# Optimization experiments

Measured on AMD Instinct MI355X. Metric: run time of the kernel, lower is better.

The kernel has to match this reference:

```python
import jax, jax.numpy as jnp
import numpy as np

TOPK = 10
NUM_CLASSES = 80
ALPHA = 1.0
BETA = 6.0
EPS = 1e-8


def setup_inputs() -> dict:
    key = jax.random.key(0)
    ks = jax.random.split(key, 6)
    B, A, NB, C = 32, 8400, 32, 80
    pred_scores = jax.random.uniform(ks[0], (B, A, C), dtype=jnp.float32)
    # anchor grid for 640x640 image, strides 8/16/32 -> 6400+1600+400 = 8400 points
    pts = []
    for s in (8, 16, 32):
        n = 640 // s
        xs = (jnp.arange(n, dtype=jnp.float32) + 0.5) * s
        gy, gx = jnp.meshgrid(xs, xs, indexing='ij')
        pts.append(jnp.stack([gx.ravel(), gy.ravel()], axis=-1))
    anchor_points = jnp.concatenate(pts, axis=0)  # (8400, 2)
    # predicted boxes: anchor point +- random extents (xyxy)
    off = jax.random.uniform(ks[1], (B, A, 4), minval=4.0, maxval=64.0, dtype=jnp.float32)
    pred_boxes = jnp.concatenate([anchor_points[None] - off[..., :2],
                                  anchor_points[None] + off[..., 2:]], axis=-1)
    gt_cxcy = jax.random.uniform(ks[2], (B, NB, 2), minval=64.0, maxval=576.0, dtype=jnp.float32)
    gt_wh = jax.random.uniform(ks[3], (B, NB, 2), minval=16.0, maxval=256.0, dtype=jnp.float32)
    gt_boxes = jnp.concatenate([gt_cxcy - gt_wh / 2, gt_cxcy + gt_wh / 2], axis=-1)
    gt_labels = jax.random.randint(ks[4], (B, NB, 1), 0, C)
    gt_mask = jax.random.uniform(ks[5], (B, NB, 1)) < 0.8  # padded-GT validity mask
    return {"pred_scores": pred_scores, "pred_boxes": pred_boxes,
            "anchor_points": anchor_points, "gt_labels": gt_labels,
            "gt_boxes": gt_boxes, "gt_mask": gt_mask}


def reference(pred_scores, pred_boxes, anchor_points, gt_labels, gt_boxes, gt_mask):
    B, A, C = pred_scores.shape
    NB = gt_boxes.shape[1]
    dt = pred_scores.dtype
    gt_valid = gt_mask[..., 0]  # (B, NB) bool

    # --- step 3 mask: anchor centers inside GT boxes ---
    lt = gt_boxes[:, :, None, :2]  # (B, NB, 1, 2)
    rb = gt_boxes[:, :, None, 2:]
    ap = anchor_points[None, None]  # (1, 1, A, 2)
    d = jnp.minimum((ap - lt).min(-1), (rb - ap).min(-1))  # (B, NB, A)
    mask_in = d > 1e-8
    valid = mask_in & gt_valid[:, :, None]
    vf = valid.astype(dt)

    # --- classification score of each anchor for each GT's class ---
    cls = gt_labels[..., 0].astype(jnp.int32)  # (B, NB)
    bcs = jnp.take_along_axis(pred_scores, cls[:, None, :], axis=2)  # (B, A, NB)
    bcs = jnp.swapaxes(bcs, 1, 2) * vf  # (B, NB, A)

    # --- pairwise IoU (xyxy) between GT and predicted boxes ---
    b1 = gt_boxes[:, :, None, :]   # (B, NB, 1, 4)
    b2 = pred_boxes[:, None, :, :]  # (B, 1, A, 4)
    iw = jnp.clip(jnp.minimum(b1[..., 2], b2[..., 2]) - jnp.maximum(b1[..., 0], b2[..., 0]), 0)
    ih = jnp.clip(jnp.minimum(b1[..., 3], b2[..., 3]) - jnp.maximum(b1[..., 1], b2[..., 1]), 0)
    inter = iw * ih
    a1 = (b1[..., 2] - b1[..., 0]) * (b1[..., 3] - b1[..., 1])
    a2 = (b2[..., 2] - b2[..., 0]) * (b2[..., 3] - b2[..., 1])
    ious = jnp.maximum(inter / (a1 + a2 - inter + 1e-10), 0.0) * vf  # (B, NB, A)

    align = jnp.power(bcs, ALPHA) * jnp.power(ious, BETA)  # (B, NB, A)

    # --- step 2: top-k candidates per GT (scatter-add counts, drop dupes) ---
    _, topk_idx = jax.lax.top_k(align, TOPK)  # (B, NB, K)
    topk_idx = jnp.where(gt_valid[:, :, None], topk_idx, 0)
    bi = jnp.arange(B)[:, None, None]
    gi = jnp.arange(NB)[None, :, None]
    counts = jnp.zeros((B, NB, A), jnp.int32).at[bi, gi, topk_idx].add(1)
    topk_mask = jnp.where(counts > 1, 0, counts).astype(dt)
    mask = topk_mask * vf  # (B, NB, A)

    # --- step 4: anchors matched to multiple GTs keep the highest-IoU GT ---
    fg = mask.sum(axis=1)  # (B, A)
    best_gt = jnp.argmax(ious, axis=1)  # (B, A)
    onehot_best = (best_gt[:, None, :] == jnp.arange(NB)[None, :, None]).astype(dt)
    mask = jnp.where(fg[:, None, :] > 1, onehot_best, mask)
    fg = mask.sum(axis=1)
    tgt_idx = jnp.argmax(mask, axis=1)  # (B, A)

    # --- gather targets ---
    target_labels = jnp.clip(jnp.take_along_axis(cls, tgt_idx, axis=1), 0, NUM_CLASSES)  # (B, A)
    target_boxes = jnp.take_along_axis(gt_boxes, tgt_idx[..., None], axis=1)  # (B, A, 4)
    target_scores = jax.nn.one_hot(target_labels, NUM_CLASSES, dtype=dt)
    target_scores = target_scores * (fg[..., None] > 0)

    # --- normalize scores by aligned metric ---
    align = align * mask
    pos_align = align.max(axis=-1, keepdims=True)           # (B, NB, 1)
    pos_iou = (ious * mask).max(axis=-1, keepdims=True)     # (B, NB, 1)
    norm = (align * pos_iou / (pos_align + EPS)).max(axis=-2)[..., None]  # (B, A, 1)
    target_scores = target_scores * norm

    return target_labels, target_boxes, target_scores, fg > 0
```

## Files before the change

kernel.cpp:

```cpp
#include <hip/hip_runtime.h>
#include <cstdint>
#include <cstddef>

#define BB 32
#define AA 8400
#define NBB 32
#define CC 80
#define TOPKN 10

typedef float nfloat4 __attribute__((ext_vector_type(4)));

__device__ __forceinline__ unsigned long long shfl_u64(unsigned long long v,
                                                       int src) {
  const int lo = __shfl((int)(v & 0xffffffffull), src, 64);
  const int hi = __shfl((int)(v >> 32), src, 64);
  return ((unsigned long long)(unsigned int)hi << 32) | (unsigned int)lo;
}

__global__ __launch_bounds__(64) void gt_topk_kernel(
    const float* __restrict__ pred_scores, const float* __restrict__ pred_boxes,
    const int* __restrict__ gt_labels, const float* __restrict__ gt_boxes,
    const int* __restrict__ gt_mask,
    int* __restrict__ tk, int* __restrict__ posA, int* __restrict__ posI,
    float* __restrict__ out) {
  const int j = blockIdx.x, b = blockIdx.y, t = threadIdx.x;
  const int g = b * NBB + j;

  if (blockIdx.z == 1) {
    const int NA = BB * AA;
    const int labels4 = NA / 4;
    const int boxes4_end = labels4 + NA;
    const int total4 = labels4 + NA + NA * 20 + NA / 4;
    nfloat4* o4 = reinterpret_cast<nfloat4*>(out);
    for (int idx = (g << 6) + t; idx < total4; idx += 1024 * 64) {
      nfloat4 v;
      if (idx < labels4) {
        const int fb = (idx * 4) / AA;
        int lab = gt_labels[fb * NBB];
        lab = min(max(lab, 0), 80);
        const float lf = (float)lab;
        v = (nfloat4){lf, lf, lf, lf};
      } else if (idx < boxes4_end) {
        const int aidx = idx - labels4;
        const int fb = aidx / AA;
        v = *reinterpret_cast<const nfloat4*>(gt_boxes + (size_t)fb * NBB * 4);
      } else {
        v = (nfloat4){0.f, 0.f, 0.f, 0.f};
      }
      __builtin_nontemporal_store(v, &o4[idx]);
    }
    return;
  }

  if (t == 0) { posA[g] = 0; posI[g] = 0; }

  const float gx0 = gt_boxes[g * 4 + 0], gy0 = gt_boxes[g * 4 + 1];
  const float gx1 = gt_boxes[g * 4 + 2], gy1 = gt_boxes[g * 4 + 3];
  const int cls = gt_labels[g];
  const bool valid = (gt_mask[g] != 0);
  const float ga1 = (gx1 - gx0) * (gy1 - gy0);

  unsigned long long tkkey[TOPKN];
#pragma unroll
  for (int k = 0; k < TOPKN; k++) tkkey[k] = 0ull;

  if (valid) {
    const int strides[3] = {8, 16, 32};
    const int grids[3] = {80, 40, 20};
    const int offs[3] = {0, 6400, 8000};
    for (int lvl = 0; lvl < 3; lvl++) {
      const float s = (float)strides[lvl];
      const int n = grids[lvl], off = offs[lvl];
      int lx = max(0, (int)floorf(gx0 / s - 0.5f) - 1);
      int hx = min(n - 1, (int)ceilf(gx1 / s - 0.5f) + 1);
      int ly = max(0, (int)floorf(gy0 / s - 0.5f) - 1);
      int hy = min(n - 1, (int)ceilf(gy1 / s - 0.5f) + 1);
      if (hx < lx || hy < ly) continue;
      const int w = hx - lx + 1;
      const int m = w * (hy - ly + 1);
      for (int i = t; i < m; i += 64) {
        const int ix = lx + i % w;
        const int iy = ly + i / w;
        const float apx = ((float)ix + 0.5f) * s;
        const float apy = ((float)iy + 0.5f) * s;
        const float d = fminf(fminf(apx - gx0, apy - gy0),
                              fminf(gx1 - apx, gy1 - apy));
        if (!(d > 1e-8f)) continue;
        const int a = off + iy * n + ix;
        const float* pb = pred_boxes + ((size_t)b * AA + a) * 4;
        const float p0 = pb[0], p1 = pb[1], p2 = pb[2], p3 = pb[3];
        const float iw = fmaxf(fminf(gx1, p2) - fmaxf(gx0, p0), 0.0f);
        const float ih = fmaxf(fminf(gy1, p3) - fmaxf(gy0, p1), 0.0f);
        const float inter = iw * ih;
        const float a2 = (p2 - p0) * (p3 - p1);
        const float iou = fmaxf(inter / (ga1 + a2 - inter + 1e-10f), 0.0f);
        const float sc = pred_scores[((size_t)b * AA + a) * CC + cls];
        const float i2 = iou * iou;
        const float align_v = sc * i2 * i2 * i2;
        const unsigned long long key =
            ((unsigned long long)__float_as_uint(align_v) << 32) |
            (unsigned int)(AA - a);
        if (key > tkkey[TOPKN - 1]) {
          tkkey[TOPKN - 1] = key;
#pragma unroll
          for (int k = TOPKN - 1; k > 0; k--) {
            if (tkkey[k] > tkkey[k - 1]) {
              unsigned long long tmp = tkkey[k];
              tkkey[k] = tkkey[k - 1];
              tkkey[k - 1] = tmp;
            }
          }
        }
      }
    }
  }

#pragma unroll
  for (int s = 1; s < 64; s <<= 1) {
    const int partner = t ^ s;
    unsigned long long other[TOPKN];
#pragma unroll
    for (int k = 0; k < TOPKN; k++) other[k] = shfl_u64(tkkey[k], partner);
    unsigned long long L[TOPKN];
#pragma unroll
    for (int k = 0; k < TOPKN; k++) {
      const unsigned long long o = other[TOPKN - 1 - k];
      L[k] = (tkkey[k] > o) ? tkkey[k] : o;
    }
#pragma unroll
    for (int r = 0; r < TOPKN; r++) {
#pragma unroll
      for (int k = (r & 1); k + 1 < TOPKN; k += 2) {
        if (L[k] < L[k + 1]) {
          const unsigned long long tmp = L[k];
          L[k] = L[k + 1];
          L[k + 1] = tmp;
        }
      }
    }
#pragma unroll
    for (int k = 0; k < TOPKN; k++) tkkey[k] = L[k];
  }

  if (t < TOPKN) {
    const unsigned long long key = tkkey[t];
    tk[g * TOPKN + t] = (key != 0ull) ? (AA - (int)(key & 0xffffffffu)) : -1;
  }
}

__global__ __launch_bounds__(64) void assign_sparse_kernel(
    const float* __restrict__ pred_scores, const float* __restrict__ pred_boxes,
    const float* __restrict__ anchor_points, const int* __restrict__ gt_labels,
    const float* __restrict__ gt_boxes, const int* __restrict__ gt_mask,
    const int* __restrict__ tk,
    int* __restrict__ resj, float* __restrict__ resAl,
    int* __restrict__ posA, int* __restrict__ posI) {
  const int j = blockIdx.x, b = blockIdx.y, t = threadIdx.x;

  __shared__ float sbox[NBB][4];
  __shared__ int scls[NBB];
  __shared__ int svalid[NBB];
  __shared__ int sa[NBB * TOPKN];

  if (t < NBB) {
    const int g = b * NBB + t;
    sbox[t][0] = gt_boxes[g * 4 + 0];
    sbox[t][1] = gt_boxes[g * 4 + 1];
    sbox[t][2] = gt_boxes[g * 4 + 2];
    sbox[t][3] = gt_boxes[g * 4 + 3];
    scls[t] = gt_labels[g];
    svalid[t] = (gt_mask[g] != 0) ? 1 : 0;
  }
  for (int e = t; e < NBB * TOPKN; e += 64) sa[e] = tk[b * NBB * TOPKN + e];
  __syncthreads();

  if (t >= TOPKN) return;
  const int a = sa[j * TOPKN + t];
  if (a < 0) return;

  int cnt = 0;
  for (int q = 0; q < NBB * TOPKN; q++) cnt += (sa[q] == a) ? 1 : 0;

  const float apx = anchor_points[a * 2 + 0];
  const float apy = anchor_points[a * 2 + 1];
  const float* pb = pred_boxes + ((size_t)b * AA + a) * 4;
  const float p0 = pb[0], p1 = pb[1], p2 = pb[2], p3 = pb[3];
  const float a2 = (p2 - p0) * (p3 - p1);

  int jj;
  float iou_f;
  if (cnt == 1) {
    jj = j;
    const float gx0 = sbox[j][0], gy0 = sbox[j][1];
    const float gx1 = sbox[j][2], gy1 = sbox[j][3];
    const float iw = fmaxf(fminf(gx1, p2) - fmaxf(gx0, p0), 0.0f);
    const float ih = fmaxf(fminf(gy1, p3) - fmaxf(gy0, p1), 0.0f);
    const float inter = iw * ih;
    const float a1 = (gx1 - gx0) * (gy1 - gy0);
    iou_f = fmaxf(inter / (a1 + a2 - inter + 1e-10f), 0.0f);
  } else {
    float best_iou = -1.0f;
    int best_j = 0;
    for (int jq = 0; jq < NBB; jq++) {
      const float gx0 = sbox[jq][0], gy0 = sbox[jq][1];
      const float gx1 = sbox[jq][2], gy1 = sbox[jq][3];
      const float d = fminf(fminf(apx - gx0, apy - gy0),
                            fminf(gx1 - apx, gy1 - apy));
      float iou = 0.0f;
      if (svalid[jq] && d > 1e-8f) {
        const float iw = fmaxf(fminf(gx1, p2) - fmaxf(gx0, p0), 0.0f);
        const float ih = fmaxf(fminf(gy1, p3) - fmaxf(gy0, p1), 0.0f);
        const float inter = iw * ih;
        const float a1 = (gx1 - gx0) * (gy1 - gy0);
        iou = fmaxf(inter / (a1 + a2 - inter + 1e-10f), 0.0f);
      }
      if (iou > best_iou) { best_iou = iou; best_j = jq; }
    }
    jj = best_j;
    iou_f = best_iou;
  }

  const float sc = pred_scores[((size_t)b * AA + a) * CC + scls[jj]];
  const float i2 = iou_f * iou_f;
  const float align_v = sc * i2 * i2 * i2;
  const int e = (b * NBB + j) * TOPKN + t;
  resj[e] = jj;
  resAl[e] = align_v;
  atomicMax(&posA[b * NBB + jj], __float_as_int(align_v));
  atomicMax(&posI[b * NBB + jj], __float_as_int(iou_f));
}

__global__ __launch_bounds__(256) void scatter_out_kernel(
    const int* __restrict__ gt_labels, const float* __restrict__ gt_boxes,
    const int* __restrict__ tk, const int* __restrict__ resj,
    const float* __restrict__ resAl, const int* __restrict__ posA,
    const int* __restrict__ posI, float* __restrict__ out) {
  const int e = blockIdx.x * 256 + threadIdx.x;
  if (e >= BB * NBB * TOPKN) return;
  const int a = tk[e];
  if (a < 0) return;
  const int b = e / (NBB * TOPKN);
  const int jj = resj[e];
  const float align_v = resAl[e];
  const float pa = __int_as_float(posA[b * NBB + jj]);
  const float pi = __int_as_float(posI[b * NBB + jj]);
  const float norm = align_v * pi / (pa + 1e-8f);
  int label = gt_labels[b * NBB + jj];
  label = min(max(label, 0), 80);
  const size_t aidx = (size_t)b * AA + a;

  out[aidx] = (float)label;
  *reinterpret_cast<float4*>(out + (size_t)BB * AA + aidx * 4) =
      *reinterpret_cast<const float4*>(gt_boxes + ((size_t)b * NBB + jj) * 4);
  if (label < CC)
    out[(size_t)BB * AA * 5 + aidx * CC + label] = norm;
  out[(size_t)BB * AA * 85 + aidx] = 1.0f;
}

extern "C" void kernel_launch(void* const* d_in, const int* in_sizes, int n_in,
                              void* d_out, int out_size, void* d_ws, size_t ws_size,
                              hipStream_t stream) {
  const float* pred_scores = (const float*)d_in[0];
  const float* pred_boxes = (const float*)d_in[1];
  const float* anchor_points = (const float*)d_in[2];
  const int* gt_labels = (const int*)d_in[3];
  const float* gt_boxes = (const float*)d_in[4];
  const int* gt_mask = (const int*)d_in[5];
  float* out = (float*)d_out;
  char* ws = (char*)d_ws;

  const size_t off_tk = 0;
  const size_t off_posA = off_tk + (size_t)BB * NBB * TOPKN * 4;
  const size_t off_posI = off_posA + 4096;
  const size_t off_resj = off_posI + 4096;
  const size_t off_resAl = off_resj + (size_t)BB * NBB * TOPKN * 4;

  int* tk = (int*)(ws + off_tk);
  int* posA = (int*)(ws + off_posA);
  int* posI = (int*)(ws + off_posI);
  int* resj = (int*)(ws + off_resj);
  float* resAl = (float*)(ws + off_resAl);

  dim3 g1(NBB, BB, 2);
  gt_topk_kernel<<<g1, 64, 0, stream>>>(pred_scores, pred_boxes, gt_labels,
                                        gt_boxes, gt_mask, tk, posA, posI,
                                        out);

  dim3 g2(NBB, BB);
  assign_sparse_kernel<<<g2, 64, 0, stream>>>(
      pred_scores, pred_boxes, anchor_points, gt_labels, gt_boxes, gt_mask,
      tk, resj, resAl, posA, posI);

  const int ncand = BB * NBB * TOPKN;
  scatter_out_kernel<<<(ncand + 255) / 256, 256, 0, stream>>>(
      gt_labels, gt_boxes, tk, resj, resAl, posA, posI, out);
}
```

Measured before the change: 48.43 us.

## Split per-GT top-k enumeration across four blocks and merge partial results

The per-GT anchor enumeration now runs over four blocks per GT, each producing a partial top-10 written to workspace, and a new merge kernel combines these into the final top-10 indices. The default output fill moves out of the fused kernel into its own kernel with 256-thread blocks. The aim is more parallelism in the enumeration phase, where one 64-thread wave per GT limited occupancy. The cost is two extra kernel launches and a round trip of partial top-k keys through global memory.

Result: slower. 97.93 us (+102.2%).

```diff
diff --git a/kernel.cpp b/kernel.cpp
--- a/kernel.cpp
+++ b/kernel.cpp
@@ -7,6 +7,7 @@
 #define NBB 32
 #define CC 80
 #define TOPKN 10
+#define ZSPLIT 4
 
 typedef float nfloat4 __attribute__((ext_vector_type(4)));
 
@@ -17,42 +18,70 @@
   return ((unsigned long long)(unsigned int)hi << 32) | (unsigned int)lo;
 }
 
-__global__ __launch_bounds__(64) void gt_topk_kernel(
+__device__ __forceinline__ void wave_merge10(unsigned long long (&tkkey)[TOPKN]) {
+#pragma unroll
+  for (int s = 1; s < 64; s <<= 1) {
+    const int partner = threadIdx.x ^ s;
+    unsigned long long other[TOPKN];
+#pragma unroll
+    for (int k = 0; k < TOPKN; k++) other[k] = shfl_u64(tkkey[k], partner);
+    unsigned long long L[TOPKN];
+#pragma unroll
+    for (int k = 0; k < TOPKN; k++) {
+      const unsigned long long o = other[TOPKN - 1 - k];
+      L[k] = (tkkey[k] > o) ? tkkey[k] : o;
+    }
+#pragma unroll
+    for (int r = 0; r < TOPKN; r++) {
+#pragma unroll
+      for (int k = (r & 1); k + 1 < TOPKN; k += 2) {
+        if (L[k] < L[k + 1]) {
+          const unsigned long long tmp = L[k];
+          L[k] = L[k + 1];
+          L[k + 1] = tmp;
+        }
+      }
+    }
+#pragma unroll
+    for (int k = 0; k < TOPKN; k++) tkkey[k] = L[k];
+  }
+}
+
+__global__ __launch_bounds__(256) void fill_default_kernel(
+    const int* __restrict__ gt_labels, const float* __restrict__ gt_boxes,
+    float* __restrict__ out) {
+  const int NA = BB * AA;
+  const int labels4 = NA / 4;
+  const int boxes4_end = labels4 + NA;
+  const int total4 = labels4 + NA + NA * 20 + NA / 4;
+  nfloat4* o4 = reinterpret_cast<nfloat4*>(out);
+  for (int idx = blockIdx.x * 256 + threadIdx.x; idx < total4;
+       idx += 1024 * 256) {
+    nfloat4 v;
+    if (idx < labels4) {
+      const int fb = (idx * 4) / AA;
+      int lab = gt_labels[fb * NBB];
+      lab = min(max(lab, 0), 80);
+      const float lf = (float)lab;
+      v = (nfloat4){lf, lf, lf, lf};
+    } else if (idx < boxes4_end) {
+      const int aidx = idx - labels4;
+      const int fb = aidx / AA;
+      v = *reinterpret_cast<const nfloat4*>(gt_boxes + (size_t)fb * NBB * 4);
+    } else {
+      v = (nfloat4){0.f, 0.f, 0.f, 0.f};
+    }
+    __builtin_nontemporal_store(v, &o4[idx]);
+  }
+}
+
+__global__ __launch_bounds__(64) void enum_part_kernel(
     const float* __restrict__ pred_scores, const float* __restrict__ pred_boxes,
     const int* __restrict__ gt_labels, const float* __restrict__ gt_boxes,
     const int* __restrict__ gt_mask,
-    int* __restrict__ tk, int* __restrict__ posA, int* __restrict__ posI,
-    float* __restrict__ out) {
-  const int j = blockIdx.x, b = blockIdx.y, t = threadIdx.x;
+    unsigned long long* __restrict__ tkpart) {
+  const int j = blockIdx.x, b = blockIdx.y, z = blockIdx.z, t = threadIdx.x;
   const int g = b * NBB + j;
-
-  if (blockIdx.z == 1) {
-    const int NA = BB * AA;
-    const int labels4 = NA / 4;
-    const int boxes4_end = labels4 + NA;
-    const int total4 = labels4 + NA + NA * 20 + NA / 4;
-    nfloat4* o4 = reinterpret_cast<nfloat4*>(out);
-    for (int idx = (g << 6) + t; idx < total4; idx += 1024 * 64) {
-      nfloat4 v;
-      if (idx < labels4) {
-        const int fb = (idx * 4) / AA;
-        int lab = gt_labels[fb * NBB];
-        lab = min(max(lab, 0), 80);
-        const float lf = (float)lab;
-        v = (nfloat4){lf, lf, lf, lf};
-      } else if (idx < boxes4_end) {
-        const int aidx = idx - labels4;
-        const int fb = aidx / AA;
-        v = *reinterpret_cast<const nfloat4*>(gt_boxes + (size_t)fb * NBB * 4);
-      } else {
-        v = (nfloat4){0.f, 0.f, 0.f, 0.f};
-      }
-      __builtin_nontemporal_store(v, &o4[idx]);
-    }
-    return;
-  }
-
-  if (t == 0) { posA[g] = 0; posI[g] = 0; }
 
   const float gx0 = gt_boxes[g * 4 + 0], gy0 = gt_boxes[g * 4 + 1];
   const float gx1 = gt_boxes[g * 4 + 2], gy1 = gt_boxes[g * 4 + 3];
@@ -78,7 +107,7 @@
       if (hx < lx || hy < ly) continue;
       const int w = hx - lx + 1;
       const int m = w * (hy - ly + 1);
-      for (int i = t; i < m; i += 64) {
+      for (int i = z * 64 + t; i < m; i += ZSPLIT * 64) {
         const int ix = lx + i % w;
         const int iy = ly + i / w;
         const float apx = ((float)ix + 0.5f) * s;
@@ -115,32 +144,28 @@
     }
   }
 
-#pragma unroll
-  for (int s = 1; s < 64; s <<= 1) {
-    const int partner = t ^ s;
-    unsigned long long other[TOPKN];
-#pragma unroll
-    for (int k = 0; k < TOPKN; k++) other[k] = shfl_u64(tkkey[k], partner);
-    unsigned long long L[TOPKN];
-#pragma unroll
-    for (int k = 0; k < TOPKN; k++) {
-      const unsigned long long o = other[TOPKN - 1 - k];
-      L[k] = (tkkey[k] > o) ? tkkey[k] : o;
-    }
-#pragma unroll
-    for (int r = 0; r < TOPKN; r++) {
-#pragma unroll
-      for (int k = (r & 1); k + 1 < TOPKN; k += 2) {
-        if (L[k] < L[k + 1]) {
-          const unsigned long long tmp = L[k];
-          L[k] = L[k + 1];
-          L[k + 1] = tmp;
-        }
-      }
-    }
-#pragma unroll
-    for (int k = 0; k < TOPKN; k++) tkkey[k] = L[k];
-  }
+  wave_merge10(tkkey);
+
+  if (t < TOPKN)
+    tkpart[((size_t)g * ZSPLIT + z) * TOPKN + t] = tkkey[t];
+}
+
+__global__ __launch_bounds__(64) void merge_topk_kernel(
+    const unsigned long long* __restrict__ tkpart,
+    int* __restrict__ tk, int* __restrict__ posA, int* __restrict__ posI) {
+  const int g = blockIdx.x, t = threadIdx.x;
+  if (t == 0) { posA[g] = 0; posI[g] = 0; }
+
+  unsigned long long tkkey[TOPKN];
+#pragma unroll
+  for (int k = 0; k < TOPKN; k++) tkkey[k] = 0ull;
+  if (t < ZSPLIT) {
+#pragma unroll
+    for (int k = 0; k < TOPKN; k++)
+      tkkey[k] = tkpart[((size_t)g * ZSPLIT + t) * TOPKN + k];
+  }
+
+  wave_merge10(tkkey);
 
   if (t < TOPKN) {
     const unsigned long long key = tkkey[t];
@@ -269,22 +294,27 @@
   float* out = (float*)d_out;
   char* ws = (char*)d_ws;
 
-  const size_t off_tk = 0;
+  const size_t off_tkpart = 0;
+  const size_t off_tk = off_tkpart + (size_t)BB * NBB * ZSPLIT * TOPKN * 8;
   const size_t off_posA = off_tk + (size_t)BB * NBB * TOPKN * 4;
   const size_t off_posI = off_posA + 4096;
   const size_t off_resj = off_posI + 4096;
   const size_t off_resAl = off_resj + (size_t)BB * NBB * TOPKN * 4;
 
+  unsigned long long* tkpart = (unsigned long long*)(ws + off_tkpart);
   int* tk = (int*)(ws + off_tk);
   int* posA = (int*)(ws + off_posA);
   int* posI = (int*)(ws + off_posI);
   int* resj = (int*)(ws + off_resj);
   float* resAl = (float*)(ws + off_resAl);
 
-  dim3 g1(NBB, BB, 2);
-  gt_topk_kernel<<<g1, 64, 0, stream>>>(pred_scores, pred_boxes, gt_labels,
-                                        gt_boxes, gt_mask, tk, posA, posI,
-                                        out);
+  fill_default_kernel<<<1024, 256, 0, stream>>>(gt_labels, gt_boxes, out);
+
+  dim3 gE(NBB, BB, ZSPLIT);
+  enum_part_kernel<<<gE, 64, 0, stream>>>(pred_scores, pred_boxes, gt_labels,
+                                          gt_boxes, gt_mask, tkpart);
+
+  merge_topk_kernel<<<BB * NBB, 64, 0, stream>>>(tkpart, tk, posA, posI);
 
   dim3 g2(NBB, BB);
   assign_sparse_kernel<<<g2, 64, 0, stream>>>(
```

## Split per-GT topk into anchor-parallel candidate compaction plus per-GT top10

Applied to the files above, without the earlier changes.

Replaces the per-GT block that scans a bounding window of anchors with an anchor-chunk-parallel kernel. Each chunk stages its score rows in shared memory, tests all 32 GTs per anchor, and appends candidate keys to per-GT lists using ballot plus atomics. A separate small kernel then picks the top 10 from each GT's list. This spreads the work across many more blocks but reads the full pred_scores tensor and adds two extra launches and a fixed candidate capacity per GT, which is a risk if more than 1536 anchors fall inside one box.

Result: slower. 90.83 us (+87.6%).

```diff
diff --git a/kernel.cpp b/kernel.cpp
--- a/kernel.cpp
+++ b/kernel.cpp
@@ -7,6 +7,10 @@
 #define NBB 32
 #define CC 80
 #define TOPKN 10
+#define MAXC 1536
+#define CSTR 16
+#define ACH 64
+#define NCH ((AA + ACH - 1) / ACH)
 
 typedef float nfloat4 __attribute__((ext_vector_type(4)));
 
@@ -17,14 +21,47 @@
   return ((unsigned long long)(unsigned int)hi << 32) | (unsigned int)lo;
 }
 
-__global__ __launch_bounds__(64) void gt_topk_kernel(
+__device__ __forceinline__ void wave_merge10(unsigned long long (&tkkey)[TOPKN]) {
+#pragma unroll
+  for (int s = 1; s < 64; s <<= 1) {
+    const int partner = threadIdx.x ^ s;
+    unsigned long long other[TOPKN];
+#pragma unroll
+    for (int k = 0; k < TOPKN; k++) other[k] = shfl_u64(tkkey[k], partner);
+    unsigned long long L[TOPKN];
+#pragma unroll
+    for (int k = 0; k < TOPKN; k++) {
+      const unsigned long long o = other[TOPKN - 1 - k];
+      L[k] = (tkkey[k] > o) ? tkkey[k] : o;
+    }
+#pragma unroll
+    for (int r = 0; r < TOPKN; r++) {
+#pragma unroll
+      for (int k = (r & 1); k + 1 < TOPKN; k += 2) {
+        if (L[k] < L[k + 1]) {
+          const unsigned long long tmp = L[k];
+          L[k] = L[k + 1];
+          L[k + 1] = tmp;
+        }
+      }
+    }
+#pragma unroll
+    for (int k = 0; k < TOPKN; k++) tkkey[k] = L[k];
+  }
+}
+
+__global__ __launch_bounds__(256) void init_cnt_kernel(int4* __restrict__ cnt4) {
+  const int i = blockIdx.x * 256 + threadIdx.x;
+  if (i < (BB * NBB * CSTR) / 4) cnt4[i] = make_int4(0, 0, 0, 0);
+}
+
+__global__ __launch_bounds__(256) void compact_fill_kernel(
     const float* __restrict__ pred_scores, const float* __restrict__ pred_boxes,
-    const int* __restrict__ gt_labels, const float* __restrict__ gt_boxes,
-    const int* __restrict__ gt_mask,
-    int* __restrict__ tk, int* __restrict__ posA, int* __restrict__ posI,
+    const float* __restrict__ anchor_points, const int* __restrict__ gt_labels,
+    const float* __restrict__ gt_boxes, const int* __restrict__ gt_mask,
+    unsigned long long* __restrict__ cand, int* __restrict__ cnt,
     float* __restrict__ out) {
-  const int j = blockIdx.x, b = blockIdx.y, t = threadIdx.x;
-  const int g = b * NBB + j;
+  const int c = blockIdx.x, b = blockIdx.y, t = threadIdx.x;
 
   if (blockIdx.z == 1) {
     const int NA = BB * AA;
@@ -32,7 +69,8 @@
     const int boxes4_end = labels4 + NA;
     const int total4 = labels4 + NA + NA * 20 + NA / 4;
     nfloat4* o4 = reinterpret_cast<nfloat4*>(out);
-    for (int idx = (g << 6) + t; idx < total4; idx += 1024 * 64) {
+    const int bid = b * NCH + c;
+    for (int idx = bid * 256 + t; idx < total4; idx += NCH * BB * 256) {
       nfloat4 v;
       if (idx < labels4) {
         const int fb = (idx * 4) / AA;
@@ -52,95 +90,120 @@
     return;
   }
 
-  if (t == 0) { posA[g] = 0; posI[g] = 0; }
-
-  const float gx0 = gt_boxes[g * 4 + 0], gy0 = gt_boxes[g * 4 + 1];
-  const float gx1 = gt_boxes[g * 4 + 2], gy1 = gt_boxes[g * 4 + 3];
-  const int cls = gt_labels[g];
-  const bool valid = (gt_mask[g] != 0);
-  const float ga1 = (gx1 - gx0) * (gy1 - gy0);
-
-  unsigned long long tkkey[TOPKN];
-#pragma unroll
-  for (int k = 0; k < TOPKN; k++) tkkey[k] = 0ull;
-
-  if (valid) {
-    const int strides[3] = {8, 16, 32};
-    const int grids[3] = {80, 40, 20};
-    const int offs[3] = {0, 6400, 8000};
-    for (int lvl = 0; lvl < 3; lvl++) {
-      const float s = (float)strides[lvl];
-      const int n = grids[lvl], off = offs[lvl];
-      int lx = max(0, (int)floorf(gx0 / s - 0.5f) - 1);
-      int hx = min(n - 1, (int)ceilf(gx1 / s - 0.5f) + 1);
-      int ly = max(0, (int)floorf(gy0 / s - 0.5f) - 1);
-      int hy = min(n - 1, (int)ceilf(gy1 / s - 0.5f) + 1);
-      if (hx < lx || hy < ly) continue;
-      const int w = hx - lx + 1;
-      const int m = w * (hy - ly + 1);
-      for (int i = t; i < m; i += 64) {
-        const int ix = lx + i % w;
-        const int iy = ly + i / w;
-        const float apx = ((float)ix + 0.5f) * s;
-        const float apy = ((float)iy + 0.5f) * s;
-        const float d = fminf(fminf(apx - gx0, apy - gy0),
-                              fminf(gx1 - apx, gy1 - apy));
-        if (!(d > 1e-8f)) continue;
-        const int a = off + iy * n + ix;
-        const float* pb = pred_boxes + ((size_t)b * AA + a) * 4;
-        const float p0 = pb[0], p1 = pb[1], p2 = pb[2], p3 = pb[3];
+  __shared__ float s_sc[ACH][CC + 1];
+  __shared__ float sbox[NBB][4];
+  __shared__ int scls[NBB];
+  __shared__ int svalid[NBB];
+
+  const int a0 = c * ACH;
+  const int nrows = min(ACH, AA - a0);
+
+  if (t < NBB) {
+    const int g = b * NBB + t;
+    sbox[t][0] = gt_boxes[g * 4 + 0];
+    sbox[t][1] = gt_boxes[g * 4 + 1];
+    sbox[t][2] = gt_boxes[g * 4 + 2];
+    sbox[t][3] = gt_boxes[g * 4 + 3];
+    scls[t] = gt_labels[g];
+    svalid[t] = (gt_mask[g] != 0) ? 1 : 0;
+  }
+
+  {
+    const float* src = pred_scores + ((size_t)b * AA + a0) * CC;
+    const int nf4 = nrows * (CC / 4);
+    for (int i = t; i < nf4; i += 256) {
+      const float4 v = reinterpret_cast<const float4*>(src)[i];
+      const int fi = i * 4;
+      const int row = fi / CC;
+      const int col = fi - row * CC;
+      s_sc[row][col + 0] = v.x;
+      s_sc[row][col + 1] = v.y;
+      s_sc[row][col + 2] = v.z;
+      s_sc[row][col + 3] = v.w;
+    }
+  }
+  __syncthreads();
+
+  if (t >= 64) return;
+
+  const bool act = (t < nrows);
+  const int a = a0 + t;
+  float apx = 0.f, apy = 0.f, p0 = 0.f, p1 = 0.f, p2 = 0.f, p3 = 0.f;
+  float a2 = 0.f;
+  if (act) {
+    apx = anchor_points[a * 2 + 0];
+    apy = anchor_points[a * 2 + 1];
+    const float* pb = pred_boxes + ((size_t)b * AA + a) * 4;
+    p0 = pb[0]; p1 = pb[1]; p2 = pb[2]; p3 = pb[3];
+    a2 = (p2 - p0) * (p3 - p1);
+  }
+  const int lane = t;
+
+  for (int j = 0; j < NBB; j++) {
+    bool hit = false;
+    float align_v = 0.0f;
+    if (act && svalid[j]) {
+      const float gx0 = sbox[j][0], gy0 = sbox[j][1];
+      const float gx1 = sbox[j][2], gy1 = sbox[j][3];
+      const float d = fminf(fminf(apx - gx0, apy - gy0),
+                            fminf(gx1 - apx, gy1 - apy));
+      if (d > 1e-8f) {
         const float iw = fmaxf(fminf(gx1, p2) - fmaxf(gx0, p0), 0.0f);
         const float ih = fmaxf(fminf(gy1, p3) - fmaxf(gy0, p1), 0.0f);
         const float inter = iw * ih;
-        const float a2 = (p2 - p0) * (p3 - p1);
-        const float iou = fmaxf(inter / (ga1 + a2 - inter + 1e-10f), 0.0f);
-        const float sc = pred_scores[((size_t)b * AA + a) * CC + cls];
+        const float a1 = (gx1 - gx0) * (gy1 - gy0);
+        const float iou = fmaxf(inter / (a1 + a2 - inter + 1e-10f), 0.0f);
+        const float s = s_sc[t][scls[j]];
         const float i2 = iou * iou;
-        const float align_v = sc * i2 * i2 * i2;
-        const unsigned long long key =
-            ((unsigned long long)__float_as_uint(align_v) << 32) |
-            (unsigned int)(AA - a);
-        if (key > tkkey[TOPKN - 1]) {
-          tkkey[TOPKN - 1] = key;
-#pragma unroll
-          for (int k = TOPKN - 1; k > 0; k--) {
-            if (tkkey[k] > tkkey[k - 1]) {
-              unsigned long long tmp = tkkey[k];
-              tkkey[k] = tkkey[k - 1];
-              tkkey[k - 1] = tmp;
-            }
-          }
+        align_v = s * i2 * i2 * i2;
+        hit = true;
+      }
+    }
+    const unsigned long long m = __ballot(hit);
+    if (m == 0ull) continue;
+    const int leader = (int)__ffsll((unsigned long long)m) - 1;
+    int base = 0;
+    if (lane == leader)
+      base = atomicAdd(&cnt[(b * NBB + j) * CSTR], (int)__popcll(m));
+    base = __shfl(base, leader);
+    if (hit) {
+      const int rank = (int)__popcll(m & ((1ull << lane) - 1ull));
+      const int pos = base + rank;
+      const unsigned long long key =
+          ((unsigned long long)__float_as_uint(align_v) << 32) |
+          (unsigned int)(AA - a);
+      cand[(size_t)(b * NBB + j) * MAXC + pos] = key;
+    }
+  }
+}
+
+__global__ __launch_bounds__(64) void top10_kernel(
+    const unsigned long long* __restrict__ cand, const int* __restrict__ cnt,
+    int* __restrict__ tk, int* __restrict__ posA, int* __restrict__ posI) {
+  const int g = blockIdx.x, t = threadIdx.x;
+  if (t == 0) { posA[g] = 0; posI[g] = 0; }
+  const int n = cnt[g * CSTR];
+
+  unsigned long long tkkey[TOPKN];
+#pragma unroll
+  for (int k = 0; k < TOPKN; k++) tkkey[k] = 0ull;
+
+  for (int i = t; i < n; i += 64) {
+    const unsigned long long key = cand[(size_t)g * MAXC + i];
+    if (key > tkkey[TOPKN - 1]) {
+      tkkey[TOPKN - 1] = key;
+#pragma unroll
+      for (int k = TOPKN - 1; k > 0; k--) {
+        if (tkkey[k] > tkkey[k - 1]) {
+          const unsigned long long tmp = tkkey[k];
+          tkkey[k] = tkkey[k - 1];
+          tkkey[k - 1] = tmp;
         }
       }
     }
   }
 
-#pragma unroll
-  for (int s = 1; s < 64; s <<= 1) {
-    const int partner = t ^ s;
-    unsigned long long other[TOPKN];
-#pragma unroll
-    for (int k = 0; k < TOPKN; k++) other[k] = shfl_u64(tkkey[k], partner);
-    unsigned long long L[TOPKN];
-#pragma unroll
-    for (int k = 0; k < TOPKN; k++) {
-      const unsigned long long o = other[TOPKN - 1 - k];
-      L[k] = (tkkey[k] > o) ? tkkey[k] : o;
-    }
-#pragma unroll
-    for (int r = 0; r < TOPKN; r++) {
-#pragma unroll
-      for (int k = (r & 1); k + 1 < TOPKN; k += 2) {
-        if (L[k] < L[k + 1]) {
-          const unsigned long long tmp = L[k];
-          L[k] = L[k + 1];
-          L[k + 1] = tmp;
-        }
-      }
-    }
-#pragma unroll
-    for (int k = 0; k < TOPKN; k++) tkkey[k] = L[k];
-  }
+  wave_merge10(tkkey);
 
   if (t < TOPKN) {
     const unsigned long long key = tkkey[t];
@@ -178,8 +241,8 @@
   const int a = sa[j * TOPKN + t];
   if (a < 0) return;
 
-  int cnt = 0;
-  for (int q = 0; q < NBB * TOPKN; q++) cnt += (sa[q] == a) ? 1 : 0;
+  int cnt_l = 0;
+  for (int q = 0; q < NBB * TOPKN; q++) cnt_l += (sa[q] == a) ? 1 : 0;
 
   const float apx = anchor_points[a * 2 + 0];
   const float apy = anchor_points[a * 2 + 1];
@@ -189,7 +252,7 @@
 
   int jj;
   float iou_f;
-  if (cnt == 1) {
+  if (cnt_l == 1) {
     jj = j;
     const float gx0 = sbox[j][0], gy0 = sbox[j][1];
     const float gx1 = sbox[j][2], gy1 = sbox[j][3];
@@ -269,22 +332,30 @@
   float* out = (float*)d_out;
   char* ws = (char*)d_ws;
 
-  const size_t off_tk = 0;
+  const size_t off_cand = 0;
+  const size_t off_cnt = off_cand + (size_t)BB * NBB * MAXC * 8;
+  const size_t off_tk = off_cnt + (size_t)BB * NBB * CSTR * 4;
   const size_t off_posA = off_tk + (size_t)BB * NBB * TOPKN * 4;
   const size_t off_posI = off_posA + 4096;
   const size_t off_resj = off_posI + 4096;
   const size_t off_resAl = off_resj + (size_t)BB * NBB * TOPKN * 4;
 
+  unsigned long long* cand = (unsigned long long*)(ws + off_cand);
+  int* cnt = (int*)(ws + off_cnt);
   int* tk = (int*)(ws + off_tk);
   int* posA = (int*)(ws + off_posA);
   int* posI = (int*)(ws + off_posI);
   int* resj = (int*)(ws + off_resj);
   float* resAl = (float*)(ws + off_resAl);
 
-  dim3 g1(NBB, BB, 2);
-  gt_topk_kernel<<<g1, 64, 0, stream>>>(pred_scores, pred_boxes, gt_labels,
-                                        gt_boxes, gt_mask, tk, posA, posI,
-                                        out);
+  init_cnt_kernel<<<16, 256, 0, stream>>>((int4*)cnt);
+
+  dim3 gC(NCH, BB, 2);
+  compact_fill_kernel<<<gC, 256, 0, stream>>>(
+      pred_scores, pred_boxes, anchor_points, gt_labels, gt_boxes, gt_mask,
+      cand, cnt, out);
+
+  top10_kernel<<<BB * NBB, 64, 0, stream>>>(cand, cnt, tk, posA, posI);
 
   dim3 g2(NBB, BB);
   assign_sparse_kernel<<<g2, 64, 0, stream>>>(
```
